# Kernel optimization log

Hardware: AMD Instinct MI355X
Metric: run time of the kernel (lower is better)

Reference implementation:

```python
import jax, jax.numpy as jnp
import numpy as np

B, S, H = 4, 1024, 1024
NH, NKV, HD = 16, 4, 64
E, TOPK, F = 8, 2, 2048
EPS = 1e-6
NEG = -1e9


def setup_inputs() -> dict:
    key = jax.random.key(0)
    ks = jax.random.split(key, 12)
    sc = lambda fan_in: 1.0 / np.sqrt(fan_in)
    x = jax.random.normal(ks[0], (B, S, H), jnp.float32)
    causal = jnp.where(jnp.tril(jnp.ones((S, S), bool)), 0.0, NEG).astype(jnp.float32)
    attention_mask = causal[None, None]  # [1,1,S,S] additive mask
    return {
        "x": x,
        "attention_mask": attention_mask,
        "w_ln1": jnp.ones((H,), jnp.float32),
        "w_ln2": jnp.ones((H,), jnp.float32),
        "Wq": jax.random.normal(ks[1], (H, NH * HD), jnp.float32) * sc(H),
        "Wk": jax.random.normal(ks[2], (H, NKV * HD), jnp.float32) * sc(H),
        "Wv": jax.random.normal(ks[3], (H, NKV * HD), jnp.float32) * sc(H),
        "Wo": jax.random.normal(ks[4], (NH * HD, H), jnp.float32) * sc(H),
        "Wgate": jax.random.normal(ks[5], (H, E), jnp.float32) * sc(H),
        "Wg": jax.random.normal(ks[6], (E, H, F), jnp.float32) * sc(H),
        "Wu": jax.random.normal(ks[7], (E, H, F), jnp.float32) * sc(H),
        "Wd": jax.random.normal(ks[8], (E, F, H), jnp.float32) * sc(F),
    }


def rmsnorm(x, w):
    var = jnp.mean(x * x, axis=-1, keepdims=True)
    return w * (x * jax.lax.rsqrt(var + EPS))


def attention(x, mask, Wq, Wk, Wv, Wo):
    b, s, _ = x.shape
    q = (x @ Wq).reshape(b, s, NH, HD).transpose(0, 2, 1, 3)   # [b,nh,s,d]
    k = (x @ Wk).reshape(b, s, NKV, HD).transpose(0, 2, 1, 3)  # [b,nkv,s,d]
    v = (x @ Wv).reshape(b, s, NKV, HD).transpose(0, 2, 1, 3)
    rep = NH // NKV
    k = jnp.repeat(k, rep, axis=1)
    v = jnp.repeat(v, rep, axis=1)
    scores = jnp.einsum("bhqd,bhkd->bhqk", q, k) / jnp.sqrt(jnp.float32(HD))
    scores = scores + mask
    attn = jax.nn.softmax(scores, axis=-1)
    out = jnp.einsum("bhqk,bhkd->bhqd", attn, v)
    out = out.transpose(0, 2, 1, 3).reshape(b, s, NH * HD)
    return out @ Wo


def moe_ffn(x, Wgate, Wg, Wu, Wd):
    b, s, h = x.shape
    xf = x.reshape(-1, h)  # [T,H]
    probs = jax.nn.softmax(xf @ Wgate, axis=-1)           # [T,E]
    topk_p, topk_i = jax.lax.top_k(probs, TOPK)            # [T,K]
    # combine weight per (token, expert): sum of routed top-k probs
    combine = jnp.sum(jax.nn.one_hot(topk_i, E, dtype=xf.dtype) * topk_p[..., None], axis=1)  # [T,E]
    gate = jax.nn.silu(jnp.einsum("th,ehf->etf", xf, Wg))
    up = jnp.einsum("th,ehf->etf", xf, Wu)
    expert_out = jnp.einsum("etf,efh->eth", gate * up, Wd)  # [E,T,H]
    out = jnp.einsum("eth,te->th", expert_out, combine)
    return out.reshape(b, s, h)


def reference(x, attention_mask, w_ln1, w_ln2, Wq, Wk, Wv, Wo, Wgate, Wg, Wu, Wd):
    h = x + attention(rmsnorm(x, w_ln1), attention_mask, Wq, Wk, Wv, Wo)
    return h + moe_ffn(rmsnorm(h, w_ln2), Wgate, Wg, Wu, Wd)
```

## Files before the change

kernel.cpp:

```cpp
#include <hip/hip_runtime.h>
#include <hip/hip_bf16.h>
#include <cstdint>

#define T_TOK    4096
#define H_DIM    1024
#define NHEAD    16
#define NKVH     4
#define HDIM     64
#define NEXP     8
#define FF       2048
#define MAXROWS  9216
#define MAXT128  72
#define NQKV     1536

typedef __attribute__((ext_vector_type(8))) short bf16x8;
typedef __attribute__((ext_vector_type(4))) short s16x4;
typedef __attribute__((ext_vector_type(4))) float f32x4;

__device__ __forceinline__ short f2bf(float f) {
  union { float f; uint32_t u; } v{f};
  uint32_t r = v.u + 0x7FFF + ((v.u >> 16) & 1);
  return (short)(r >> 16);
}
__device__ __forceinline__ float bf2f(short h) {
  union { uint32_t u; float f; } v;
  v.u = ((uint32_t)(unsigned short)h) << 16;
  return v.f;
}

__device__ __forceinline__ void async_copy16(const void* g, void* l) {
  __builtin_amdgcn_global_load_lds(
      (const __attribute__((address_space(1))) unsigned int*)g,
      (__attribute__((address_space(3))) unsigned int*)l, 16, 0, 0);
}

__global__ __launch_bounds__(256) void rmsnorm3_kernel(
    const float* __restrict__ x, const float* __restrict__ w,
    float* __restrict__ out32, short* __restrict__ out3, short* __restrict__ outb,
    const float* __restrict__ Wgate, float* __restrict__ topk_p,
    int* __restrict__ topk_i) {
  int t = blockIdx.x, tid = threadIdx.x;
  const float4 xv = *(const float4*)(x + (size_t)t * H_DIM + tid * 4);
  float ss = xv.x * xv.x + xv.y * xv.y + xv.z * xv.z + xv.w * xv.w;
#pragma unroll
  for (int off = 32; off > 0; off >>= 1) ss += __shfl_down(ss, off);
  __shared__ float red[4];
  __shared__ float gred[4][8];
  if ((tid & 63) == 0) red[tid >> 6] = ss;
  __syncthreads();
  float tot = red[0] + red[1] + red[2] + red[3];
  float rs = rsqrtf(tot * (1.0f / 1024.0f) + 1e-6f);
  const float4 wv = *(const float4*)(w + tid * 4);
  float vals[4];
  vals[0] = xv.x * rs * wv.x; vals[1] = xv.y * rs * wv.y;
  vals[2] = xv.z * rs * wv.z; vals[3] = xv.w * rs * wv.w;
  if (out32) {
    float4 o; o.x = vals[0]; o.y = vals[1]; o.z = vals[2]; o.w = vals[3];
    *(float4*)(out32 + (size_t)t * H_DIM + tid * 4) = o;
  }
  if (out3) {
    union { short s[4]; uint2 u; } H, L;
#pragma unroll
    for (int i = 0; i < 4; ++i) {
      H.s[i] = f2bf(vals[i]);
      L.s[i] = f2bf(vals[i] - bf2f(H.s[i]));
    }
    size_t base = (size_t)t * 3072 + tid * 4;
    *(uint2*)(out3 + base) = H.u;
    *(uint2*)(out3 + base + 1024) = L.u;
    *(uint2*)(out3 + base + 2048) = H.u;
  }
  if (outb) {
    union { short s[4]; uint2 u; } Hb;
#pragma unroll
    for (int i = 0; i < 4; ++i) Hb.s[i] = f2bf(vals[i]);
    *(uint2*)(outb + (size_t)t * H_DIM + tid * 4) = Hb.u;
  }
  if (Wgate) {
    float a[8] = {};
#pragma unroll
    for (int j = 0; j < 4; ++j) {
      const float4 w0 = *(const float4*)(Wgate + (size_t)(tid * 4 + j) * 8);
      const float4 w1 = *(const float4*)(Wgate + (size_t)(tid * 4 + j) * 8 + 4);
      a[0] += vals[j] * w0.x; a[1] += vals[j] * w0.y;
      a[2] += vals[j] * w0.z; a[3] += vals[j] * w0.w;
      a[4] += vals[j] * w1.x; a[5] += vals[j] * w1.y;
      a[6] += vals[j] * w1.z; a[7] += vals[j] * w1.w;
    }
#pragma unroll
    for (int e = 0; e < 8; ++e)
#pragma unroll
      for (int off = 32; off > 0; off >>= 1) a[e] += __shfl_down(a[e], off);
    if ((tid & 63) == 0) {
#pragma unroll
      for (int e = 0; e < 8; ++e) gred[tid >> 6][e] = a[e];
    }
    __syncthreads();
    if (tid == 0) {
      float p[8];
#pragma unroll
      for (int e = 0; e < 8; ++e)
        p[e] = gred[0][e] + gred[1][e] + gred[2][e] + gred[3][e];
      float m = p[0];
#pragma unroll
      for (int e = 1; e < 8; ++e) m = fmaxf(m, p[e]);
      float s = 0.0f;
#pragma unroll
      for (int e = 0; e < 8; ++e) { p[e] = __expf(p[e] - m); s += p[e]; }
      float invs = 1.0f / s;
#pragma unroll
      for (int e = 0; e < 8; ++e) p[e] *= invs;
      int i1 = 0;
#pragma unroll
      for (int e = 1; e < 8; ++e) if (p[e] > p[i1]) i1 = e;
      int i2 = (i1 == 0) ? 1 : 0;
#pragma unroll
      for (int e = 0; e < 8; ++e) if (e != i1 && p[e] > p[i2]) i2 = e;
      topk_i[t * 2] = i1;     topk_p[t * 2] = p[i1];
      topk_i[t * 2 + 1] = i2; topk_p[t * 2 + 1] = p[i2];
    }
  }
}

__global__ __launch_bounds__(256) void conv_qkvo(
    const float* __restrict__ Wq, const float* __restrict__ Wk,
    const float* __restrict__ Wv, const float* __restrict__ Wo,
    short* __restrict__ Wqkv3t, short* __restrict__ Wo3t) {
  __shared__ float t[32][33];
  int bx = blockIdx.x;
  const float* W; short* dst; int N, nb;
  if (bx < 32)      { W = Wq; dst = Wqkv3t;                         N = 1024; nb = bx; }
  else if (bx < 40) { W = Wk; dst = Wqkv3t + (size_t)1024 * 3072;   N = 256;  nb = bx - 32; }
  else if (bx < 48) { W = Wv; dst = Wqkv3t + (size_t)1280 * 3072;   N = 256;  nb = bx - 40; }
  else              { W = Wo; dst = Wo3t;                           N = 1024; nb = bx - 48; }
  int n0 = nb * 32, k0 = blockIdx.y * 32;
  int tx = threadIdx.x & 7, ty = threadIdx.x >> 3;
  float4 v = *(const float4*)(W + (size_t)(k0 + ty) * N + n0 + tx * 4);
  t[ty][tx * 4 + 0] = v.x; t[ty][tx * 4 + 1] = v.y;
  t[ty][tx * 4 + 2] = v.z; t[ty][tx * 4 + 3] = v.w;
  __syncthreads();
  union { short s[4]; uint2 u; } H, L;
#pragma unroll
  for (int i = 0; i < 4; ++i) {
    float f = t[tx * 4 + i][ty];
    H.s[i] = f2bf(f);
    L.s[i] = f2bf(f - bf2f(H.s[i]));
  }
  size_t base = (size_t)(n0 + ty) * 3072 + k0 + tx * 4;
  *(uint2*)(dst + base) = H.u;
  *(uint2*)(dst + base + 1024) = H.u;
  *(uint2*)(dst + base + 2048) = L.u;
}

__global__ __launch_bounds__(256) void conv_gud(
    const float* __restrict__ Wg, const float* __restrict__ Wu, const float* __restrict__ Wd,
    short* __restrict__ Wg_t, short* __restrict__ Wu_t, short* __restrict__ Wd_t) {
  __shared__ float t[32][33];
  const int z = blockIdx.z, e = z & 7, which = z >> 3;
  const int bx = blockIdx.x;
  const float* Wsrc; short* dst; int K, N, n0, k0;
  const size_t es = (size_t)e * 1024 * 2048;
  if (which == 0)      { Wsrc = Wg + es; dst = Wg_t + es; K = 1024; N = 2048; n0 = (bx & 63) * 32; k0 = (bx >> 6) * 32; }
  else if (which == 1) { Wsrc = Wu + es; dst = Wu_t + es; K = 1024; N = 2048; n0 = (bx & 63) * 32; k0 = (bx >> 6) * 32; }
  else                 { Wsrc = Wd + es; dst = Wd_t + es; K = 2048; N = 1024; n0 = (bx & 31) * 32; k0 = (bx >> 5) * 32; }
  int tx = threadIdx.x & 7, ty = threadIdx.x >> 3;
  float4 v = *(const float4*)(Wsrc + (size_t)(k0 + ty) * N + n0 + tx * 4);
  t[ty][tx * 4 + 0] = v.x; t[ty][tx * 4 + 1] = v.y;
  t[ty][tx * 4 + 2] = v.z; t[ty][tx * 4 + 3] = v.w;
  __syncthreads();
  union { short s[4]; uint2 u; } H;
#pragma unroll
  for (int i = 0; i < 4; ++i) H.s[i] = f2bf(t[tx * 4 + i][ty]);
  *(uint2*)(dst + (size_t)(n0 + ty) * K + k0 + tx * 4) = H.u;
}

__global__ __launch_bounds__(256) void kv_pre(
    const float* __restrict__ qkv,
    short* __restrict__ k2g, short* __restrict__ v2g) {
  __shared__ __align__(16) short K2[64 * 128];
  __shared__ __align__(16) short V2[64 * 128];
  const int blk = blockIdx.x;
  const int kt = blk & 15, bk = blk >> 4;
  const int b = bk >> 2, kvh = bk & 3;
  const int tid = threadIdx.x;
  {
    const int skey = tid >> 2, sdq = tid & 3;
    const float* kr = qkv + (size_t)(b * 1024 + kt * 64 + skey) * NQKV + 1024 + kvh * 64 + sdq * 16;
    float4 f[4];
    f[0] = *(const float4*)(kr); f[1] = *(const float4*)(kr + 4);
    f[2] = *(const float4*)(kr + 8); f[3] = *(const float4*)(kr + 12);
    short* krow = K2 + skey * 128;
#pragma unroll
    for (int c2 = 0; c2 < 2; ++c2) {
      float e[8];
      e[0]=f[2*c2].x; e[1]=f[2*c2].y; e[2]=f[2*c2].z; e[3]=f[2*c2].w;
      e[4]=f[2*c2+1].x; e[5]=f[2*c2+1].y; e[6]=f[2*c2+1].z; e[7]=f[2*c2+1].w;
      union { short s[8]; s16x4 v4[2]; } Hh, Ll;
#pragma unroll
      for (int i = 0; i < 8; ++i) {
        Hh.s[i] = f2bf(e[i]);
        Ll.s[i] = f2bf(e[i] - bf2f(Hh.s[i]));
      }
      int ch = 2 * sdq + c2;
      int hc = (ch ^ (skey & 15)) * 8;
      int lc = ((8 + ch) ^ (skey & 15)) * 8;
      *(s16x4*)&krow[hc] = Hh.v4[0]; *(s16x4*)&krow[hc + 4] = Hh.v4[1];
      *(s16x4*)&krow[lc] = Ll.v4[0]; *(s16x4*)&krow[lc + 4] = Ll.v4[1];
    }
  }
  {
    const int sp = tid >> 3, sdg = tid & 7;
    const float* vr0 = qkv + (size_t)(b * 1024 + kt * 64 + 2 * sp) * NQKV + 1280 + kvh * 64 + sdg * 8;
    const float* vr1 = vr0 + NQKV;
    float4 a0 = *(const float4*)(vr0), a1 = *(const float4*)(vr0 + 4);
    float4 b0 = *(const float4*)(vr1), b1 = *(const float4*)(vr1 + 4);
    float va[8], vb[8];
    va[0]=a0.x; va[1]=a0.y; va[2]=a0.z; va[3]=a0.w; va[4]=a1.x; va[5]=a1.y; va[6]=a1.z; va[7]=a1.w;
    vb[0]=b0.x; vb[1]=b0.y; vb[2]=b0.z; vb[3]=b0.w; vb[4]=b1.x; vb[5]=b1.y; vb[6]=b1.z; vb[7]=b1.w;
    int ch = sp >> 2, di = (sp & 3) * 2;
#pragma unroll
    for (int i = 0; i < 8; ++i) {
      int d = sdg * 8 + i;
      short h0 = f2bf(va[i]), l0 = f2bf(va[i] - bf2f(h0));
      short h1 = f2bf(vb[i]), l1 = f2bf(vb[i] - bf2f(h1));
      uint32_t hp = (uint32_t)(uint16_t)h0 | ((uint32_t)(uint16_t)h1 << 16);
      uint32_t lp = (uint32_t)(uint16_t)l0 | ((uint32_t)(uint16_t)l1 << 16);
      short* vrow = V2 + d * 128;
      *(uint32_t*)&vrow[(ch ^ (d & 15)) * 8 + di] = hp;
      *(uint32_t*)&vrow[((8 + ch) ^ (d & 15)) * 8 + di] = lp;
    }
  }
  __syncthreads();
  uint4* kd = (uint4*)(k2g + (size_t)blk * 8192);
  uint4* vd = (uint4*)(v2g + (size_t)blk * 8192);
  const uint4* ks = (const uint4*)K2;
  const uint4* vs = (const uint4*)V2;
#pragma unroll
  for (int i = 0; i < 4; ++i) {
    kd[tid + i * 256] = ks[tid + i * 256];
    vd[tid + i * 256] = vs[tid + i * 256];
  }
}

__global__ __launch_bounds__(256, 2) void gemm_bf16(
    const short* __restrict__ A, const short* __restrict__ Bt,
    const float* __restrict__ Res, float* __restrict__ C,
    int N, int K, const int* __restrict__ tile_expert, long long expert_stride) {
  __shared__ short As[8192];
  __shared__ short Bs[8192];
  const int tid = threadIdx.x;
  const int w = tid >> 6, lane = tid & 63;
  const int row0 = blockIdx.y * 128, col0 = blockIdx.x * 128;
  if (tile_expert) {
    int e = tile_expert[blockIdx.y];
    if (e < 0) return;
    Bt += (size_t)e * expert_stride;
  }
  const int wm = (w & 1) * 64, wn = (w >> 1) * 64;
  const int lcol = lane & 15, quad = lane >> 4;
  const int cbase = w * 256;
  f32x4 acc[4][4];
#pragma unroll
  for (int i = 0; i < 4; ++i)
#pragma unroll
    for (int j = 0; j < 4; ++j) acc[i][j] = (f32x4){0.f, 0.f, 0.f, 0.f};

  for (int k0 = 0; k0 < K; k0 += 64) {
#pragma unroll
    for (int i = 0; i < 4; ++i) {
      int c = cbase + i * 64 + lane;
      int r = c >> 3, cp = c & 7;
      int sc = (cp ^ (r & 7)) * 8;
      async_copy16(A + (size_t)(row0 + r) * K + k0 + sc, As + (size_t)(cbase + i * 64) * 8);
      async_copy16(Bt + (size_t)(col0 + r) * K + k0 + sc, Bs + (size_t)(cbase + i * 64) * 8);
    }
    __syncthreads();
#pragma unroll
    for (int step = 0; step < 2; ++step) {
      bf16x8 a[4], b[4];
#pragma unroll
      for (int t = 0; t < 4; ++t) {
        int m = wm + t * 16 + lcol;
        int q = quad + step * 4;
        a[t] = *(const bf16x8*)&As[(m * 8 + (q ^ (m & 7))) * 8];
        int n = wn + t * 16 + lcol;
        b[t] = *(const bf16x8*)&Bs[(n * 8 + (q ^ (n & 7))) * 8];
      }
#pragma unroll
      for (int mt = 0; mt < 4; ++mt)
#pragma unroll
        for (int nt = 0; nt < 4; ++nt)
          acc[mt][nt] = __builtin_amdgcn_mfma_f32_16x16x32_bf16(a[mt], b[nt], acc[mt][nt], 0, 0, 0);
    }
    __syncthreads();
  }
#pragma unroll
  for (int mt = 0; mt < 4; ++mt)
#pragma unroll
    for (int r = 0; r < 4; ++r) {
      int gr = row0 + wm + mt * 16 + quad * 4 + r;
#pragma unroll
      for (int nt = 0; nt < 4; ++nt) {
        int gc = col0 + wn + nt * 16 + lcol;
        float v = acc[mt][nt][r];
        if (Res) v += Res[(size_t)gr * N + gc];
        C[(size_t)gr * N + gc] = v;
      }
    }
}

__global__ __launch_bounds__(256, 2) void moe_gemm1_bf16(
    const short* __restrict__ hnb, const int* __restrict__ pair_token,
    const short* __restrict__ Bgt, const short* __restrict__ But,
    const int* __restrict__ tile_expert, short* __restrict__ act) {
  __shared__ short As[8192];
  __shared__ short Bgs[8192];
  __shared__ short Bus[8192];
  const int tid = threadIdx.x;
  const int w = tid >> 6, lane = tid & 63;
  const int row0 = blockIdx.y * 128, col0 = blockIdx.x * 128;
  int e = tile_expert[blockIdx.y];
  if (e < 0) return;
  const short* Bg = Bgt + (size_t)e * (FF * H_DIM);
  const short* Bu = But + (size_t)e * (FF * H_DIM);
  const int wm = (w & 1) * 64, wn = (w >> 1) * 64;
  const int lcol = lane & 15, quad = lane >> 4;
  const int cbase = w * 256;
  const int K = H_DIM;
  int toki[4];
#pragma unroll
  for (int i = 0; i < 4; ++i) {
    int c = cbase + i * 64 + lane;
    int tk = pair_token[row0 + (c >> 3)];
    toki[i] = ((unsigned)tk <= 4095u) ? tk : 0;
  }
  f32x4 accg[4][4], accu[4][4];
#pragma unroll
  for (int i = 0; i < 4; ++i)
#pragma unroll
    for (int j = 0; j < 4; ++j) {
      accg[i][j] = (f32x4){0.f, 0.f, 0.f, 0.f};
      accu[i][j] = (f32x4){0.f, 0.f, 0.f, 0.f};
    }
  for (int k0 = 0; k0 < K; k0 += 64) {
#pragma unroll
    for (int i = 0; i < 4; ++i) {
      int c = cbase + i * 64 + lane;
      int r = c >> 3, cp = c & 7;
      int sc = (cp ^ (r & 7)) * 8;
      async_copy16(hnb + (size_t)toki[i] * H_DIM + k0 + sc, As + (size_t)(cbase + i * 64) * 8);
      async_copy16(Bg + (size_t)(col0 + r) * K + k0 + sc, Bgs + (size_t)(cbase + i * 64) * 8);
      async_copy16(Bu + (size_t)(col0 + r) * K + k0 + sc, Bus + (size_t)(cbase + i * 64) * 8);
    }
    __syncthreads();
#pragma unroll
    for (int step = 0; step < 2; ++step) {
      bf16x8 a[4], bg[4], bu[4];
#pragma unroll
      for (int t = 0; t < 4; ++t) {
        int m = wm + t * 16 + lcol;
        int q = quad + step * 4;
        a[t] = *(const bf16x8*)&As[(m * 8 + (q ^ (m & 7))) * 8];
        int n = wn + t * 16 + lcol;
        bg[t] = *(const bf16x8*)&Bgs[(n * 8 + (q ^ (n & 7))) * 8];
        bu[t] = *(const bf16x8*)&Bus[(n * 8 + (q ^ (n & 7))) * 8];
      }
#pragma unroll
      for (int mt = 0; mt < 4; ++mt)
#pragma unroll
        for (int nt = 0; nt < 4; ++nt) {
          accg[mt][nt] = __builtin_amdgcn_mfma_f32_16x16x32_bf16(a[mt], bg[nt], accg[mt][nt], 0, 0, 0);
          accu[mt][nt] = __builtin_amdgcn_mfma_f32_16x16x32_bf16(a[mt], bu[nt], accu[mt][nt], 0, 0, 0);
        }
    }
    __syncthreads();
  }
#pragma unroll
  for (int mt = 0; mt < 4; ++mt)
#pragma unroll
    for (int r = 0; r < 4; ++r) {
      int gr = row0 + wm + mt * 16 + quad * 4 + r;
#pragma unroll
      for (int nt = 0; nt < 4; ++nt) {
        int gc = col0 + wn + nt * 16 + lcol;
        float g = accg[mt][nt][r], u = accu[mt][nt][r];
        float val = (g * u) / (1.0f + __expf(-g));
        act[(size_t)gr * FF + gc] = f2bf(val);
      }
    }
}

__global__ __launch_bounds__(256, 3) void attn_kernel(
    const float* __restrict__ q, const short* __restrict__ k2g,
    const short* __restrict__ v2g, short* __restrict__ aout3) {
  const int QTMAP[16] = {0, 15, 1, 14, 2, 13, 3, 12, 4, 11, 5, 10, 6, 9, 7, 8};
  const int bh = blockIdx.x & 63;
  const int qt = QTMAP[blockIdx.x >> 6];
  const int b = bh >> 4, h = bh & 15, kvh = h >> 2;
  __shared__ __align__(16) short K2[64 * 128];
  __shared__ __align__(16) short V2[64 * 128];
  __shared__ short P2[4 * 16 * 136];
  const int tid = threadIdx.x;
  const int w = tid >> 6, lane = tid & 63;
  const int lcol = lane & 15, quad = lane >> 4;

  const float* qrow = q + (size_t)(b * 1024 + qt * 64 + w * 16 + lcol) * NQKV + h * 64;
  union { short s[8]; bf16x8 v; } qhi0, qhi1, qlo0, qlo1;
  {
    float e0[8], e1[8];
    float4 f0 = *(const float4*)(qrow + quad * 8);
    float4 f1 = *(const float4*)(qrow + quad * 8 + 4);
    float4 f2 = *(const float4*)(qrow + 32 + quad * 8);
    float4 f3 = *(const float4*)(qrow + 32 + quad * 8 + 4);
    e0[0]=f0.x; e0[1]=f0.y; e0[2]=f0.z; e0[3]=f0.w; e0[4]=f1.x; e0[5]=f1.y; e0[6]=f1.z; e0[7]=f1.w;
    e1[0]=f2.x; e1[1]=f2.y; e1[2]=f2.z; e1[3]=f2.w; e1[4]=f3.x; e1[5]=f3.y; e1[6]=f3.z; e1[7]=f3.w;
#pragma unroll
    for (int i = 0; i < 8; ++i) {
      qhi0.s[i] = f2bf(e0[i]); qlo0.s[i] = f2bf(e0[i] - bf2f(qhi0.s[i]));
      qhi1.s[i] = f2bf(e1[i]); qlo1.s[i] = f2bf(e1[i] - bf2f(qhi1.s[i]));
    }
  }
  f32x4 O[4];
#pragma unroll
  for (int i = 0; i < 4; ++i) O[i] = (f32x4){0.f, 0.f, 0.f, 0.f};
  float m_i[4] = {-1e30f, -1e30f, -1e30f, -1e30f};
  float l_i[4] = {0.f, 0.f, 0.f, 0.f};

  const size_t tbase = (size_t)((b * 4 + kvh) * 16);
  short* p2w = P2 + w * (16 * 136);

  for (int kt = 0; kt <= qt; ++kt) {
    __syncthreads();
    {
      const short* ksrc = k2g + (tbase + kt) * 8192;
      const short* vsrc = v2g + (tbase + kt) * 8192;
      const int wb = w * 2048;
#pragma unroll
      for (int i = 0; i < 4; ++i) {
        async_copy16(ksrc + wb + i * 512 + lane * 8, K2 + wb + i * 512);
        async_copy16(vsrc + wb + i * 512 + lane * 8, V2 + wb + i * 512);
      }
    }
    __syncthreads();
    f32x4 S[4];
#pragma unroll
    for (int nt = 0; nt < 4; ++nt) {
      S[nt] = (f32x4){0.f, 0.f, 0.f, 0.f};
      const short* krow = K2 + (nt * 16 + lcol) * 128;
      bf16x8 kh0 = *(const bf16x8*)&krow[(quad ^ lcol) * 8];
      bf16x8 kh1 = *(const bf16x8*)&krow[((4 + quad) ^ lcol) * 8];
      bf16x8 kl0 = *(const bf16x8*)&krow[((8 + quad) ^ lcol) * 8];
      bf16x8 kl1 = *(const bf16x8*)&krow[((12 + quad) ^ lcol) * 8];
      S[nt] = __builtin_amdgcn_mfma_f32_16x16x32_bf16(qhi0.v, kh0, S[nt], 0, 0, 0);
      S[nt] = __builtin_amdgcn_mfma_f32_16x16x32_bf16(qhi1.v, kh1, S[nt], 0, 0, 0);
      S[nt] = __builtin_amdgcn_mfma_f32_16x16x32_bf16(qlo0.v, kh0, S[nt], 0, 0, 0);
      S[nt] = __builtin_amdgcn_mfma_f32_16x16x32_bf16(qlo1.v, kh1, S[nt], 0, 0, 0);
      S[nt] = __builtin_amdgcn_mfma_f32_16x16x32_bf16(qhi0.v, kl0, S[nt], 0, 0, 0);
      S[nt] = __builtin_amdgcn_mfma_f32_16x16x32_bf16(qhi1.v, kl1, S[nt], 0, 0, 0);
    }
    const bool diag = (kt == qt);
#pragma unroll
    for (int r = 0; r < 4; ++r) {
      float sv[4];
#pragma unroll
      for (int nt = 0; nt < 4; ++nt) sv[nt] = S[nt][r] * 0.125f;
      if (diag) {
        int rl = w * 16 + quad * 4 + r;
#pragma unroll
        for (int nt = 0; nt < 4; ++nt)
          if (nt * 16 + lcol > rl) sv[nt] = -1e30f;
      }
      float mx = fmaxf(fmaxf(sv[0], sv[1]), fmaxf(sv[2], sv[3]));
      mx = fmaxf(mx, __shfl_xor(mx, 1));
      mx = fmaxf(mx, __shfl_xor(mx, 2));
      mx = fmaxf(mx, __shfl_xor(mx, 4));
      mx = fmaxf(mx, __shfl_xor(mx, 8));
      float m_new = fmaxf(m_i[r], mx);
      float pe[4], rs = 0.f;
#pragma unroll
      for (int nt = 0; nt < 4; ++nt) { pe[nt] = __expf(sv[nt] - m_new); rs += pe[nt]; }
      rs += __shfl_xor(rs, 1);
      rs += __shfl_xor(rs, 2);
      rs += __shfl_xor(rs, 4);
      rs += __shfl_xor(rs, 8);
      float alpha = __expf(m_i[r] - m_new);
      l_i[r] = l_i[r] * alpha + rs;
      m_i[r] = m_new;
      O[0][r] *= alpha; O[1][r] *= alpha; O[2][r] *= alpha; O[3][r] *= alpha;
      short* prow = p2w + (quad * 4 + r) * 136;
#pragma unroll
      for (int nt = 0; nt < 4; ++nt) {
        short hb = f2bf(pe[nt]);
        prow[nt * 16 + lcol] = hb;
        prow[64 + nt * 16 + lcol] = f2bf(pe[nt] - bf2f(hb));
      }
    }
    {
      const short* pr = p2w + lcol * 136;
      bf16x8 ph0 = *(const bf16x8*)&pr[quad * 8];
      bf16x8 ph1 = *(const bf16x8*)&pr[32 + quad * 8];
      bf16x8 pl0 = *(const bf16x8*)&pr[64 + quad * 8];
      bf16x8 pl1 = *(const bf16x8*)&pr[96 + quad * 8];
#pragma unroll
      for (int nt = 0; nt < 4; ++nt) {
        const short* vrow = V2 + (nt * 16 + lcol) * 128;
        bf16x8 vh0 = *(const bf16x8*)&vrow[(quad ^ lcol) * 8];
        bf16x8 vh1 = *(const bf16x8*)&vrow[((4 + quad) ^ lcol) * 8];
        bf16x8 vl0 = *(const bf16x8*)&vrow[((8 + quad) ^ lcol) * 8];
        bf16x8 vl1 = *(const bf16x8*)&vrow[((12 + quad) ^ lcol) * 8];
        O[nt] = __builtin_amdgcn_mfma_f32_16x16x32_bf16(ph0, vh0, O[nt], 0, 0, 0);
        O[nt] = __builtin_amdgcn_mfma_f32_16x16x32_bf16(ph1, vh1, O[nt], 0, 0, 0);
        O[nt] = __builtin_amdgcn_mfma_f32_16x16x32_bf16(pl0, vh0, O[nt], 0, 0, 0);
        O[nt] = __builtin_amdgcn_mfma_f32_16x16x32_bf16(pl1, vh1, O[nt], 0, 0, 0);
        O[nt] = __builtin_amdgcn_mfma_f32_16x16x32_bf16(ph0, vl0, O[nt], 0, 0, 0);
        O[nt] = __builtin_amdgcn_mfma_f32_16x16x32_bf16(ph1, vl1, O[nt], 0, 0, 0);
      }
    }
  }
#pragma unroll
  for (int r = 0; r < 4; ++r) {
    float inv = 1.0f / l_i[r];
    size_t tok = (size_t)(b * 1024 + qt * 64 + w * 16 + quad * 4 + r);
#pragma unroll
    for (int nt = 0; nt < 4; ++nt) {
      float val = O[nt][r] * inv;
      short hb = f2bf(val);
      short lb = f2bf(val - bf2f(hb));
      size_t tb = tok * 3072 + h * 64 + nt * 16 + lcol;
      aout3[tb] = hb;
      aout3[tb + 1024] = lb;
      aout3[tb + 2048] = hb;
    }
  }
}

__global__ __launch_bounds__(256) void moe_route(
    const int* __restrict__ topk_i, int* __restrict__ pair_token,
    int* __restrict__ slot_idx, int* __restrict__ tile_expert) {
  __shared__ int hist[8];
  __shared__ int segs[9];
  __shared__ int cur[8];
  const int tid = threadIdx.x;
  int cnt[8] = {};
  for (int idx = tid; idx < T_TOK * 2; idx += 256) cnt[topk_i[idx]]++;
  if (tid < 8) hist[tid] = 0;
  __syncthreads();
#pragma unroll
  for (int e = 0; e < 8; ++e)
    if (cnt[e]) atomicAdd(&hist[e], cnt[e]);
  __syncthreads();
  if (tid == 0) {
    int off = 0;
    for (int e = 0; e < 8; ++e) {
      segs[e] = off; cur[e] = off;
      off += (hist[e] + 127) & ~127;
    }
    segs[8] = off;
    for (int i = 0; i < MAXT128; ++i) {
      int row = i * 128, e = -1;
      for (int x = 0; x < 8; ++x)
        if (row >= segs[x] && row < segs[x + 1]) e = x;
      tile_expert[i] = e;
    }
  }
  __syncthreads();
  for (int idx = tid; idx < T_TOK * 2; idx += 256) {
    int e = topk_i[idx];
    int slot = atomicAdd(&cur[e], 1);
    pair_token[slot] = idx >> 1;
    slot_idx[idx] = slot;
  }
}

__global__ __launch_bounds__(256) void final_combine(
    const float* __restrict__ hbuf, const float* __restrict__ pair_out,
    const int* __restrict__ slot_idx, const float* __restrict__ topk_p,
    float* __restrict__ out) {
  int t = blockIdx.x, d = threadIdx.x;
  int s0 = slot_idx[t * 2], s1 = slot_idx[t * 2 + 1];
  float p0 = topk_p[t * 2], p1 = topk_p[t * 2 + 1];
  float4 hv = *(const float4*)(hbuf + (size_t)t * 1024 + d * 4);
  float4 a = *(const float4*)(pair_out + (size_t)s0 * 1024 + d * 4);
  float4 b = *(const float4*)(pair_out + (size_t)s1 * 1024 + d * 4);
  float4 o;
  o.x = hv.x + p0 * a.x + p1 * b.x;
  o.y = hv.y + p0 * a.y + p1 * b.y;
  o.z = hv.z + p0 * a.z + p1 * b.z;
  o.w = hv.w + p0 * a.w + p1 * b.w;
  *(float4*)(out + (size_t)t * 1024 + d * 4) = o;
}

extern "C" void kernel_launch(void* const* d_in, const int* in_sizes, int n_in,
                              void* d_out, int out_size, void* d_ws, size_t ws_size,
                              hipStream_t stream) {
  const float* x     = (const float*)d_in[0];
  const float* w_ln1 = (const float*)d_in[2];
  const float* w_ln2 = (const float*)d_in[3];
  const float* Wq    = (const float*)d_in[4];
  const float* Wk    = (const float*)d_in[5];
  const float* Wv    = (const float*)d_in[6];
  const float* Wo    = (const float*)d_in[7];
  const float* Wgate = (const float*)d_in[8];
  const float* Wg    = (const float*)d_in[9];
  const float* Wu    = (const float*)d_in[10];
  const float* Wd    = (const float*)d_in[11];
  float* out = (float*)d_out;

  char* base = (char*)d_ws;
  const size_t SZ_XN3   = (size_t)T_TOK * 3072 * 2;
  const size_t SZ_WQKV3 = (size_t)NQKV * 3072 * 2;
  const size_t SZ_QKV   = (size_t)T_TOK * NQKV * 4;
  short* xn3  = (short*)base;
  short* k2g = (short*)base;
  short* v2g = (short*)(base + (size_t)4194304);
  short* Wqkv3t = (short*)(base + SZ_XN3);
  float* qkv = (float*)(base + SZ_XN3 + SZ_WQKV3);
  float* pair_out = (float*)base;
  size_t offB = SZ_XN3 + SZ_WQKV3 + SZ_QKV;
  short* act   = (short*)(base + offB);
  short* aout3 = (short*)(base + offB + (size_t)8388608);
  short* Wo3t  = (short*)(base + offB + (size_t)8388608 + SZ_XN3);
  size_t off2 = offB + (size_t)8388608 + SZ_XN3 + (size_t)1024 * 3072 * 2;
  float* hbuf = (float*)(base + off2);                 off2 += (size_t)T_TOK * 1024 * 4;
  short* hnb  = (short*)(base + off2);                 off2 += (size_t)T_TOK * 1024 * 2;
  short* Wg_t = (short*)(base + off2);                 off2 += (size_t)NEXP * H_DIM * FF * 2;
  short* Wu_t = (short*)(base + off2);                 off2 += (size_t)NEXP * H_DIM * FF * 2;
  short* Wd_t = (short*)(base + off2);                 off2 += (size_t)NEXP * H_DIM * FF * 2;
  float* topk_p = (float*)(base + off2);               off2 += (size_t)T_TOK * 2 * 4;
  int* topk_i      = (int*)(base + off2);              off2 += (size_t)T_TOK * 2 * 4;
  int* slot_idx    = (int*)(base + off2);              off2 += (size_t)T_TOK * 2 * 4;
  int* pair_token  = (int*)(base + off2);              off2 += (size_t)MAXROWS * 4;
  int* tile_expert = (int*)(base + off2);              off2 += 512;

  conv_qkvo<<<dim3(80, 32), 256, 0, stream>>>(Wq, Wk, Wv, Wo, Wqkv3t, Wo3t);
  conv_gud<<<dim3(2048, 1, 24), 256, 0, stream>>>(Wg, Wu, Wd, Wg_t, Wu_t, Wd_t);

  rmsnorm3_kernel<<<T_TOK, 256, 0, stream>>>(x, w_ln1, nullptr, xn3, nullptr,
                                             nullptr, nullptr, nullptr);
  gemm_bf16<<<dim3(12, 32), 256, 0, stream>>>(xn3, Wqkv3t, nullptr, qkv, NQKV, 3072, nullptr, 0);
  kv_pre<<<dim3(256), 256, 0, stream>>>(qkv, k2g, v2g);
  attn_kernel<<<dim3(1024), 256, 0, stream>>>(qkv, k2g, v2g, aout3);
  gemm_bf16<<<dim3(8, 32), 256, 0, stream>>>(aout3, Wo3t, x, hbuf, 1024, 3072, nullptr, 0);
  rmsnorm3_kernel<<<T_TOK, 256, 0, stream>>>(hbuf, w_ln2, nullptr, nullptr, hnb,
                                             Wgate, topk_p, topk_i);
  moe_route<<<1, 256, 0, stream>>>(topk_i, pair_token, slot_idx, tile_expert);
  moe_gemm1_bf16<<<dim3(16, MAXT128), 256, 0, stream>>>(hnb, pair_token, Wg_t, Wu_t,
                                                        tile_expert, act);
  gemm_bf16<<<dim3(8, MAXT128), 256, 0, stream>>>(act, Wd_t, nullptr, pair_out, 1024, 2048,
                                                  tile_expert, (long long)FF * H_DIM);
  final_combine<<<T_TOK, 256, 0, stream>>>(hbuf, pair_out, slot_idx, topk_p, out);
}
```

Before: 682.1 us.

## Fuse MoE combine into down-proj GEMM epilogue via weighted atomic scatter-add

The MoE down-projection GEMM now scales each output row by its routing probability and atomically adds it straight into the final output, keyed by pair_token. This removes the final_combine kernel and the intermediate pair_out buffer. The residual is seeded by having the second rmsnorm kernel copy hbuf into out. The cost is fp32 atomics (two per output element), which make the summation order nondeterministic, plus clearing the pair arrays inside moe_route.

Measured after the change: 693.0 us. No clear change (+1.6%).

```diff
diff --git a/kernel.cpp b/kernel.cpp
--- a/kernel.cpp
+++ b/kernel.cpp
@@ -38,9 +38,10 @@
     const float* __restrict__ x, const float* __restrict__ w,
     float* __restrict__ out32, short* __restrict__ out3, short* __restrict__ outb,
     const float* __restrict__ Wgate, float* __restrict__ topk_p,
-    int* __restrict__ topk_i) {
+    int* __restrict__ topk_i, float* __restrict__ outcp) {
   int t = blockIdx.x, tid = threadIdx.x;
   const float4 xv = *(const float4*)(x + (size_t)t * H_DIM + tid * 4);
+  if (outcp) *(float4*)(outcp + (size_t)t * H_DIM + tid * 4) = xv;
   float ss = xv.x * xv.x + xv.y * xv.y + xv.z * xv.z + xv.w * xv.w;
 #pragma unroll
   for (int off = 32; off > 0; off >>= 1) ss += __shfl_down(ss, off);
@@ -245,17 +246,12 @@
 __global__ __launch_bounds__(256, 2) void gemm_bf16(
     const short* __restrict__ A, const short* __restrict__ Bt,
     const float* __restrict__ Res, float* __restrict__ C,
-    int N, int K, const int* __restrict__ tile_expert, long long expert_stride) {
+    int N, int K) {
   __shared__ short As[8192];
   __shared__ short Bs[8192];
   const int tid = threadIdx.x;
   const int w = tid >> 6, lane = tid & 63;
   const int row0 = blockIdx.y * 128, col0 = blockIdx.x * 128;
-  if (tile_expert) {
-    int e = tile_expert[blockIdx.y];
-    if (e < 0) return;
-    Bt += (size_t)e * expert_stride;
-  }
   const int wm = (w & 1) * 64, wn = (w >> 1) * 64;
   const int lcol = lane & 15, quad = lane >> 4;
   const int cbase = w * 256;
@@ -390,6 +386,76 @@
     }
 }
 
+__global__ __launch_bounds__(256, 2) void moe_gemm2_bf16(
+    const short* __restrict__ A, const short* __restrict__ Bt,
+    const int* __restrict__ tile_expert, const int* __restrict__ pair_token,
+    const float* __restrict__ pair_p, float* __restrict__ out) {
+  __shared__ short As[8192];
+  __shared__ short Bs[8192];
+  const int tid = threadIdx.x;
+  const int w = tid >> 6, lane = tid & 63;
+  const int row0 = blockIdx.y * 128, col0 = blockIdx.x * 128;
+  int e = tile_expert[blockIdx.y];
+  if (e < 0) return;
+  Bt += (size_t)e * ((size_t)FF * H_DIM);
+  const int wm = (w & 1) * 64, wn = (w >> 1) * 64;
+  const int lcol = lane & 15, quad = lane >> 4;
+  const int cbase = w * 256;
+  const int K = FF, N = H_DIM;
+  f32x4 acc[4][4];
+#pragma unroll
+  for (int i = 0; i < 4; ++i)
+#pragma unroll
+    for (int j = 0; j < 4; ++j) acc[i][j] = (f32x4){0.f, 0.f, 0.f, 0.f};
+
+  for (int k0 = 0; k0 < K; k0 += 64) {
+#pragma unroll
+    for (int i = 0; i < 4; ++i) {
+      int c = cbase + i * 64 + lane;
+      int r = c >> 3, cp = c & 7;
+      int sc = (cp ^ (r & 7)) * 8;
+      async_copy16(A + (size_t)(row0 + r) * K + k0 + sc, As + (size_t)(cbase + i * 64) * 8);
+      async_copy16(Bt + (size_t)(col0 + r) * K + k0 + sc, Bs + (size_t)(cbase + i * 64) * 8);
+    }
+    __syncthreads();
+#pragma unroll
+    for (int step = 0; step < 2; ++step) {
+      bf16x8 a[4], b[4];
+#pragma unroll
+      for (int t = 0; t < 4; ++t) {
+        int m = wm + t * 16 + lcol;
+        int q = quad + step * 4;
+        a[t] = *(const bf16x8*)&As[(m * 8 + (q ^ (m & 7))) * 8];
+        int n = wn + t * 16 + lcol;
+        b[t] = *(const bf16x8*)&Bs[(n * 8 + (q ^ (n & 7))) * 8];
+      }
+#pragma unroll
+      for (int mt = 0; mt < 4; ++mt)
+#pragma unroll
+        for (int nt = 0; nt < 4; ++nt)
+          acc[mt][nt] = __builtin_amdgcn_mfma_f32_16x16x32_bf16(a[mt], b[nt], acc[mt][nt], 0, 0, 0);
+    }
+    __syncthreads();
+  }
+#pragma unroll
+  for (int mt = 0; mt < 4; ++mt) {
+    int gr0 = row0 + wm + mt * 16 + quad * 4;
+#pragma unroll
+    for (int r = 0; r < 4; ++r) {
+      int gr = gr0 + r;
+      int tok = pair_token[gr];
+      float wgt = pair_p[gr];
+      if ((unsigned)tok <= 4095u && wgt != 0.f) {
+#pragma unroll
+        for (int nt = 0; nt < 4; ++nt) {
+          int gc = col0 + wn + nt * 16 + lcol;
+          atomicAdd(&out[(size_t)tok * H_DIM + gc], wgt * acc[mt][nt][r]);
+        }
+      }
+    }
+  }
+}
+
 __global__ __launch_bounds__(256, 3) void attn_kernel(
     const float* __restrict__ q, const short* __restrict__ k2g,
     const short* __restrict__ v2g, short* __restrict__ aout3) {
@@ -535,12 +601,14 @@
 }
 
 __global__ __launch_bounds__(256) void moe_route(
-    const int* __restrict__ topk_i, int* __restrict__ pair_token,
-    int* __restrict__ slot_idx, int* __restrict__ tile_expert) {
+    const int* __restrict__ topk_i, const float* __restrict__ topk_p,
+    int* __restrict__ pair_token, float* __restrict__ pair_p,
+    int* __restrict__ tile_expert) {
   __shared__ int hist[8];
   __shared__ int segs[9];
   __shared__ int cur[8];
   const int tid = threadIdx.x;
+  for (int i = tid; i < MAXROWS; i += 256) { pair_p[i] = 0.f; pair_token[i] = -1; }
   int cnt[8] = {};
   for (int idx = tid; idx < T_TOK * 2; idx += 256) cnt[topk_i[idx]]++;
   if (tid < 8) hist[tid] = 0;
@@ -568,26 +636,8 @@
     int e = topk_i[idx];
     int slot = atomicAdd(&cur[e], 1);
     pair_token[slot] = idx >> 1;
-    slot_idx[idx] = slot;
-  }
-}
-
-__global__ __launch_bounds__(256) void final_combine(
-    const float* __restrict__ hbuf, const float* __restrict__ pair_out,
-    const int* __restrict__ slot_idx, const float* __restrict__ topk_p,
-    float* __restrict__ out) {
-  int t = blockIdx.x, d = threadIdx.x;
-  int s0 = slot_idx[t * 2], s1 = slot_idx[t * 2 + 1];
-  float p0 = topk_p[t * 2], p1 = topk_p[t * 2 + 1];
-  float4 hv = *(const float4*)(hbuf + (size_t)t * 1024 + d * 4);
-  float4 a = *(const float4*)(pair_out + (size_t)s0 * 1024 + d * 4);
-  float4 b = *(const float4*)(pair_out + (size_t)s1 * 1024 + d * 4);
-  float4 o;
-  o.x = hv.x + p0 * a.x + p1 * b.x;
-  o.y = hv.y + p0 * a.y + p1 * b.y;
-  o.z = hv.z + p0 * a.z + p1 * b.z;
-  o.w = hv.w + p0 * a.w + p1 * b.w;
-  *(float4*)(out + (size_t)t * 1024 + d * 4) = o;
+    pair_p[slot] = topk_p[idx];
+  }
 }
 
 extern "C" void kernel_launch(void* const* d_in, const int* in_sizes, int n_in,
@@ -615,7 +665,6 @@
   short* v2g = (short*)(base + (size_t)4194304);
   short* Wqkv3t = (short*)(base + SZ_XN3);
   float* qkv = (float*)(base + SZ_XN3 + SZ_WQKV3);
-  float* pair_out = (float*)base;
   size_t offB = SZ_XN3 + SZ_WQKV3 + SZ_QKV;
   short* act   = (short*)(base + offB);
   short* aout3 = (short*)(base + offB + (size_t)8388608);
@@ -628,7 +677,7 @@
   short* Wd_t = (short*)(base + off2);                 off2 += (size_t)NEXP * H_DIM * FF * 2;
   float* topk_p = (float*)(base + off2);               off2 += (size_t)T_TOK * 2 * 4;
   int* topk_i      = (int*)(base + off2);              off2 += (size_t)T_TOK * 2 * 4;
-  int* slot_idx    = (int*)(base + off2);              off2 += (size_t)T_TOK * 2 * 4;
+  float* pair_p    = (float*)(base + off2);            off2 += (size_t)MAXROWS * 4;
   int* pair_token  = (int*)(base + off2);              off2 += (size_t)MAXROWS * 4;
   int* tile_expert = (int*)(base + off2);              off2 += 512;
 
@@ -636,17 +685,16 @@
   conv_gud<<<dim3(2048, 1, 24), 256, 0, stream>>>(Wg, Wu, Wd, Wg_t, Wu_t, Wd_t);
 
   rmsnorm3_kernel<<<T_TOK, 256, 0, stream>>>(x, w_ln1, nullptr, xn3, nullptr,
-                                             nullptr, nullptr, nullptr);
-  gemm_bf16<<<dim3(12, 32), 256, 0, stream>>>(xn3, Wqkv3t, nullptr, qkv, NQKV, 3072, nullptr, 0);
+                                             nullptr, nullptr, nullptr, nullptr);
+  gemm_bf16<<<dim3(12, 32), 256, 0, stream>>>(xn3, Wqkv3t, nullptr, qkv, NQKV, 3072);
   kv_pre<<<dim3(256), 256, 0, stream>>>(qkv, k2g, v2g);
   attn_kernel<<<dim3(1024), 256, 0, stream>>>(qkv, k2g, v2g, aout3);
-  gemm_bf16<<<dim3(8, 32), 256, 0, stream>>>(aout3, Wo3t, x, hbuf, 1024, 3072, nullptr, 0);
+  gemm_bf16<<<dim3(8, 32), 256, 0, stream>>>(aout3, Wo3t, x, hbuf, 1024, 3072);
   rmsnorm3_kernel<<<T_TOK, 256, 0, stream>>>(hbuf, w_ln2, nullptr, nullptr, hnb,
-                                             Wgate, topk_p, topk_i);
-  moe_route<<<1, 256, 0, stream>>>(topk_i, pair_token, slot_idx, tile_expert);
+                                             Wgate, topk_p, topk_i, out);
+  moe_route<<<1, 256, 0, stream>>>(topk_i, topk_p, pair_token, pair_p, tile_expert);
   moe_gemm1_bf16<<<dim3(16, MAXT128), 256, 0, stream>>>(hnb, pair_token, Wg_t, Wu_t,
                                                         tile_expert, act);
-  gemm_bf16<<<dim3(8, MAXT128), 256, 0, stream>>>(act, Wd_t, nullptr, pair_out, 1024, 2048,
-                                                  tile_expert, (long long)FF * H_DIM);
-  final_combine<<<T_TOK, 256, 0, stream>>>(hbuf, pair_out, slot_idx, topk_p, out);
-}
+  moe_gemm2_bf16<<<dim3(8, MAXT128), 256, 0, stream>>>(act, Wd_t, tile_expert,
+                                                       pair_token, pair_p, out);
+}
```
